# Optimization experiments

Hardware: AMD Instinct MI355X
Metric: run time of the kernel (lower is better)

Reference implementation:

```python
import jax, jax.numpy as jnp
import numpy as np

D_MODEL = 512
N = 2048
BS = 8


def setup_inputs() -> dict:
    key = jax.random.key(0)
    ks = jax.random.split(key, 5)
    inputs1 = jax.random.normal(ks[0], (BS, N, D_MODEL), dtype=jnp.float32)
    inputs2 = jax.random.normal(ks[1], (BS, N, D_MODEL), dtype=jnp.float32)
    # torch Linear weights: init.normal_(std=0.001), bias=0
    Wq = 0.001 * jax.random.normal(ks[2], (D_MODEL, D_MODEL), dtype=jnp.float32)
    Wk = 0.001 * jax.random.normal(ks[3], (D_MODEL, D_MODEL), dtype=jnp.float32)
    Wv = 0.001 * jax.random.normal(ks[4], (D_MODEL, D_MODEL), dtype=jnp.float32)
    bq = jnp.zeros((D_MODEL,), dtype=jnp.float32)
    bk = jnp.zeros((D_MODEL,), dtype=jnp.float32)
    bv = jnp.zeros((D_MODEL,), dtype=jnp.float32)
    # nn.Parameter(torch.ones((n, n)))
    position_biases = jnp.ones((N, N), dtype=jnp.float32)
    return {"inputs1": inputs1, "inputs2": inputs2, "Wq": Wq, "bq": bq,
            "Wk": Wk, "bk": bk, "Wv": Wv, "bv": bv,
            "position_biases": position_biases}


def reference(inputs1, inputs2, Wq, bq, Wk, bk, Wv, bv, position_biases):
    # torch Linear: y = x @ W.T + b
    q = inputs1 @ Wq.T + bq                     # [b, n, d]
    k = inputs1 @ Wk.T + bk                     # [b, s, d]
    v = inputs2 @ Wv.T + bv                     # [b, s, d]
    # exp(k[b,s,d] + bias[t,s]) = exp(bias)[t,s] * exp(k)[b,s,d] -> separable,
    # avoiding the original's (n, bs, n, dim) broadcast intermediate.
    expB = jnp.exp(position_biases)             # [t, s]
    ek = jnp.exp(k)                             # [b, s, d]
    num = jnp.einsum('ts,bsd->btd', expB, ek * v)
    den = jnp.einsum('ts,bsd->btd', expB, ek)
    return jax.nn.sigmoid(q) * (num / den)      # [b, n, d]
```

## Files before the change

### kernel.cpp

```cpp
#include <hip/hip_runtime.h>

typedef float  f32x4  __attribute__((ext_vector_type(4)));
typedef __bf16 bf16x8 __attribute__((ext_vector_type(8)));
typedef __bf16 bf16x4 __attribute__((ext_vector_type(4)));
typedef __bf16 bf16x2 __attribute__((ext_vector_type(2)));

#define D_MODEL 512
#define SEQ     2048
#define BATCH   8
#define ROWS    (BATCH * SEQ)

#define ASYNC_COPY16(dst_lds, src_glb)                                          \
  __builtin_amdgcn_global_load_lds(                                             \
      (const __attribute__((address_space(1))) void*)(src_glb),                 \
      (__attribute__((address_space(3))) void*)(dst_lds), 16, 0, 0)

__global__ void cvt_all_kernel(const float* __restrict__ x1,
                               const float* __restrict__ x2,
                               const float* __restrict__ posb,
                               const float* __restrict__ Wq,
                               const float* __restrict__ Wk,
                               const float* __restrict__ Wv,
                               const float* __restrict__ bq,
                               const float* __restrict__ bk,
                               const float* __restrict__ bv,
                               __bf16* __restrict__ x1b, __bf16* __restrict__ x2b,
                               __bf16* __restrict__ expBb, __bf16* __restrict__ wb,
                               float* __restrict__ bcat)
{
  const int blk = blockIdx.x;
  if (blk < 16384) {
    const float* in = (blk < 8192) ? x1 : x2;
    __bf16* out = (blk < 8192) ? x1b : x2b;
    const int i = (blk & 8191) * 256 + threadIdx.x;
    float4 v = ((const float4*)in)[i];
    bf16x4 o = { (__bf16)v.x, (__bf16)v.y, (__bf16)v.z, (__bf16)v.w };
    ((bf16x4*)out)[i] = o;
  } else if (blk < 20480) {
    const int i = (blk - 16384) * 256 + threadIdx.x;
    float4 v = ((const float4*)posb)[i];
    bf16x4 o = { (__bf16)__expf(v.x), (__bf16)__expf(v.y),
                 (__bf16)__expf(v.z), (__bf16)__expf(v.w) };
    ((bf16x4*)expBb)[i] = o;
  } else if (blk < 21248) {
    const int i = (blk - 20480) * 256 + threadIdx.x;
    const int nW4 = D_MODEL * D_MODEL / 4;
    const float* src = (i < nW4) ? Wq : (i < 2 * nW4) ? Wk : Wv;
    const int ii = i - ((i < nW4) ? 0 : (i < 2 * nW4) ? nW4 : 2 * nW4);
    float4 v = ((const float4*)src)[ii];
    bf16x4 o = { (__bf16)v.x, (__bf16)v.y, (__bf16)v.z, (__bf16)v.w };
    ((bf16x4*)wb)[i] = o;
  } else {
    const int t = (blk - 21248) * 256 + threadIdx.x;
    float v = (t < 512) ? bq[t] : (t < 1024) ? bk[t - 512] : bv[t - 1024];
    bcat[t] = v;
  }
}

__global__ __launch_bounds__(256) void qkv_gemm_kernel(
    const __bf16* __restrict__ x1b, const __bf16* __restrict__ x2b,
    const __bf16* __restrict__ wb, const float* __restrict__ bcat,
    __bf16* __restrict__ sigq, __bf16* __restrict__ kb,
    __bf16* __restrict__ vb)
{
  __shared__ __align__(16) __bf16 As[128 * 64];
  __shared__ __align__(16) __bf16 Bs[128 * 64];

  const int K = D_MODEL;
  const int tid  = threadIdx.x;
  const int wave = tid >> 6;
  const int lane = tid & 63;
  const int quad = lane >> 4;
  const int l16  = lane & 15;
  const int wm   = (wave >> 1) * 64;
  const int wn   = (wave & 1) * 64;
  const int m0 = blockIdx.x * 128;
  const int n0 = blockIdx.y * 128;
  const int l8r = lane >> 3;
  const int scol = ((lane & 7) ^ l8r) * 8;

  const __bf16* A = (blockIdx.y < 8) ? x1b : x2b;

  const __bf16* ga[4]; const __bf16* gb[4];
  __bf16* la[4]; __bf16* lb[4];
  #pragma unroll
  for (int i = 0; i < 4; ++i) {
    ga[i] = A  + (long long)(m0 + i * 32 + wave * 8 + l8r) * K + scol;
    gb[i] = wb + (long long)(n0 + i * 32 + wave * 8 + l8r) * K + scol;
    la[i] = As + (i * 32 + wave * 8) * 64;
    lb[i] = Bs + (i * 32 + wave * 8) * 64;
  }

  f32x4 acc[4][4];
  #pragma unroll
  for (int i = 0; i < 4; ++i)
    #pragma unroll
    for (int j = 0; j < 4; ++j) acc[i][j] = (f32x4){0.f, 0.f, 0.f, 0.f};

  for (int k0 = 0; k0 < K; k0 += 64) {
    #pragma unroll
    for (int i = 0; i < 4; ++i) {
      ASYNC_COPY16(la[i], ga[i] + k0);
      ASYNC_COPY16(lb[i], gb[i] + k0);
    }
    __syncthreads();
    #pragma unroll
    for (int kk = 0; kk < 2; ++kk) {
      const int slot = ((quad + kk * 4) ^ (l16 & 7)) * 8;
      bf16x8 af[4], bfr[4];
      #pragma unroll
      for (int i = 0; i < 4; ++i)
        af[i] = *(const bf16x8*)&As[(wm + i * 16 + l16) * 64 + slot];
      #pragma unroll
      for (int j = 0; j < 4; ++j)
        bfr[j] = *(const bf16x8*)&Bs[(wn + j * 16 + l16) * 64 + slot];
      #pragma unroll
      for (int i = 0; i < 4; ++i)
        #pragma unroll
        for (int j = 0; j < 4; ++j)
          acc[i][j] = __builtin_amdgcn_mfma_f32_16x16x32_bf16(af[i], bfr[j],
                                                              acc[i][j], 0, 0, 0);
    }
    __syncthreads();
  }

  #pragma unroll
  for (int j = 0; j < 4; ++j) {
    const int col = n0 + wn + j * 16 + l16;
    const float bvv = bcat[col];
    #pragma unroll
    for (int i = 0; i < 4; ++i) {
      #pragma unroll
      for (int r = 0; r < 4; ++r) {
        const int row = m0 + wm + i * 16 + quad * 4 + r;
        float x = acc[i][j][r] + bvv;
        if (col < D_MODEL) {
          sigq[(long long)row * D_MODEL + col] = (__bf16)(1.f / (1.f + __expf(-x)));
        } else if (col < 2 * D_MODEL) {
          kb[(long long)row * D_MODEL + (col - D_MODEL)] = (__bf16)x;
        } else {
          vb[(long long)row * D_MODEL + (col - 2 * D_MODEL)] = (__bf16)x;
        }
      }
    }
  }
}

__global__ __launch_bounds__(256) void transform_transpose_kernel(
    const __bf16* __restrict__ kb, const __bf16* __restrict__ vb,
    __bf16* __restrict__ ekvT)
{
  __shared__ float t_ekv[64][67];
  __shared__ float t_ek[64][67];
  const int b  = blockIdx.z;
  const int s0 = blockIdx.x * 64;
  const int d0 = blockIdx.y * 64;
  const int tx = threadIdx.x;
  const int ty = threadIdx.y;
  const __bf16* kp = kb + (long long)b * SEQ * D_MODEL;
  const __bf16* vp = vb + (long long)b * SEQ * D_MODEL;

  #pragma unroll
  for (int it = 0; it < 8; ++it) {
    const int sl = ty + it * 8;
    const long long base = (long long)(s0 + sl) * D_MODEL + d0 + 2 * tx;
    bf16x2 kk2 = *(const bf16x2*)(kp + base);
    bf16x2 vv2 = *(const bf16x2*)(vp + base);
    float e0 = __expf((float)kk2[0]);
    float e1 = __expf((float)kk2[1]);
    t_ek[sl][2 * tx]      = e0;
    t_ek[sl][2 * tx + 1]  = e1;
    t_ekv[sl][2 * tx]     = e0 * (float)vv2[0];
    t_ekv[sl][2 * tx + 1] = e1 * (float)vv2[1];
  }
  __syncthreads();

  __bf16* outp = ekvT + (long long)b * (2 * D_MODEL) * SEQ;
  #pragma unroll
  for (int it = 0; it < 8; ++it) {
    const int dl = ty + it * 8;
    const int d  = d0 + dl;
    const int gr = (d >> 5) * 64 + (d & 31);
    bf16x2 ev = { (__bf16)t_ekv[2 * tx][dl], (__bf16)t_ekv[2 * tx + 1][dl] };
    bf16x2 ee = { (__bf16)t_ek[2 * tx][dl],  (__bf16)t_ek[2 * tx + 1][dl] };
    *(bf16x2*)(outp + (long long)gr * SEQ + s0 + 2 * tx)        = ev;
    *(bf16x2*)(outp + (long long)(gr + 32) * SEQ + s0 + 2 * tx) = ee;
  }
}

__global__ __launch_bounds__(256) void einsum_fused_kernel(
    const __bf16* __restrict__ A, const __bf16* __restrict__ BtAll,
    const __bf16* __restrict__ sigq, float* __restrict__ out)
{
  __shared__ __align__(16) __bf16 As[128 * 64];
  __shared__ __align__(16) __bf16 Bs[128 * 64];

  const int b = blockIdx.z;
  const __bf16* Bt = BtAll + (long long)b * (2 * D_MODEL) * SEQ;
  const int K = SEQ;

  const int tid  = threadIdx.x;
  const int wave = tid >> 6;
  const int lane = tid & 63;
  const int quad = lane >> 4;
  const int l16  = lane & 15;
  const int wm   = (wave >> 1) * 64;
  const int wn   = (wave & 1) * 64;
  const int m0 = blockIdx.x * 128;
  const int n0 = blockIdx.y * 128;
  const int l8r = lane >> 3;
  const int scol = ((lane & 7) ^ l8r) * 8;

  const __bf16* ga[4]; const __bf16* gb[4];
  __bf16* la[4]; __bf16* lb[4];
  #pragma unroll
  for (int i = 0; i < 4; ++i) {
    ga[i] = A  + (long long)(m0 + i * 32 + wave * 8 + l8r) * K + scol;
    gb[i] = Bt + (long long)(n0 + i * 32 + wave * 8 + l8r) * K + scol;
    la[i] = As + (i * 32 + wave * 8) * 64;
    lb[i] = Bs + (i * 32 + wave * 8) * 64;
  }

  f32x4 acc[4][4];
  #pragma unroll
  for (int i = 0; i < 4; ++i)
    #pragma unroll
    for (int j = 0; j < 4; ++j) acc[i][j] = (f32x4){0.f, 0.f, 0.f, 0.f};

  for (int k0 = 0; k0 < K; k0 += 64) {
    #pragma unroll
    for (int i = 0; i < 4; ++i) {
      ASYNC_COPY16(la[i], ga[i] + k0);
      ASYNC_COPY16(lb[i], gb[i] + k0);
    }
    __syncthreads();

    #pragma unroll
    for (int kk = 0; kk < 2; ++kk) {
      const int slot = ((quad + kk * 4) ^ (l16 & 7)) * 8;
      bf16x8 af[4], bfr[4];
      #pragma unroll
      for (int i = 0; i < 4; ++i)
        af[i] = *(const bf16x8*)&As[(wm + i * 16 + l16) * 64 + slot];
      #pragma unroll
      for (int j = 0; j < 4; ++j)
        bfr[j] = *(const bf16x8*)&Bs[(wn + j * 16 + l16) * 64 + slot];
      #pragma unroll
      for (int i = 0; i < 4; ++i)
        #pragma unroll
        for (int j = 0; j < 4; ++j)
          acc[i][j] = __builtin_amdgcn_mfma_f32_16x16x32_bf16(af[i], bfr[j],
                                                              acc[i][j], 0, 0, 0);
    }
    __syncthreads();
  }

  const int g = (n0 + wn) >> 6;
  #pragma unroll
  for (int j = 0; j < 2; ++j) {
    const int d = g * 32 + j * 16 + l16;
    #pragma unroll
    for (int i = 0; i < 4; ++i) {
      #pragma unroll
      for (int r = 0; r < 4; ++r) {
        const int row = m0 + wm + i * 16 + quad * 4 + r;
        const long long off = ((long long)b * SEQ + row) * D_MODEL + d;
        const float num = acc[i][j][r];
        const float den = acc[i][j + 2][r];
        out[off] = (float)sigq[off] * (num / den);
      }
    }
  }
}

extern "C" void kernel_launch(void* const* d_in, const int* in_sizes, int n_in,
                              void* d_out, int out_size, void* d_ws, size_t ws_size,
                              hipStream_t stream) {
  const float* inputs1 = (const float*)d_in[0];
  const float* inputs2 = (const float*)d_in[1];
  const float* Wq = (const float*)d_in[2];
  const float* bq = (const float*)d_in[3];
  const float* Wk = (const float*)d_in[4];
  const float* bk = (const float*)d_in[5];
  const float* Wv = (const float*)d_in[6];
  const float* bv = (const float*)d_in[7];
  const float* posb = (const float*)d_in[8];
  float* out = (float*)d_out;

  char* ws = (char*)d_ws;
  const long long szX  = (long long)ROWS * D_MODEL * 2;
  const long long szW  = (long long)D_MODEL * D_MODEL * 2;
  const long long szEB = (long long)SEQ * SEQ * 2;
  const long long szT  = (long long)BATCH * 2 * D_MODEL * SEQ * 2;
  __bf16* x1b   = (__bf16*)(ws);                 ws += szX;
  __bf16* x2b   = (__bf16*)(ws);                 ws += szX;
  __bf16* wb    = (__bf16*)(ws);                 ws += 3 * szW;
  float*  bcat  = (float*)(ws);                  ws += 3 * D_MODEL * 4;
  __bf16* expBb = (__bf16*)(ws);                 ws += szEB;
  __bf16* sigq  = (__bf16*)(ws);                 ws += szX;
  __bf16* kb    = (__bf16*)(ws);                 ws += szX;
  __bf16* vb    = (__bf16*)(ws);                 ws += szX;
  __bf16* ekvT  = (__bf16*)(ws);                 ws += szT;

  cvt_all_kernel<<<21254, 256, 0, stream>>>(inputs1, inputs2, posb,
                                            Wq, Wk, Wv, bq, bk, bv,
                                            x1b, x2b, expBb, wb, bcat);

  {
    dim3 g(ROWS / 128, (3 * D_MODEL) / 128, 1);
    qkv_gemm_kernel<<<g, 256, 0, stream>>>(x1b, x2b, wb, bcat, sigq, kb, vb);
  }

  {
    dim3 g(SEQ / 64, D_MODEL / 64, BATCH);
    dim3 blk(32, 8, 1);
    transform_transpose_kernel<<<g, blk, 0, stream>>>(kb, vb, ekvT);
  }

  {
    dim3 g(SEQ / 128, (2 * D_MODEL) / 128, BATCH);
    einsum_fused_kernel<<<g, 256, 0, stream>>>(expBb, ekvT, sigq, out);
  }
}
```

Before: 270.5 us.

## Compute K and V projections transposed in GEMM, replace transpose kernel with streaming combine

The QKV GEMM is restructured so that K and V are computed as W·X^T, which writes them directly in a [d, rows] transposed layout. This lets the shared-memory transpose kernel be replaced by a simple vectorized elementwise combine that computes exp(k) and exp(k)*v. Each GEMM block now handles two tiles, with the next tile's first stage prefetched across the tile boundary. Biases are read directly and the separate bias-concatenation pass is dropped. The trade-off is that the transposed epilogue writes are strided 2-byte stores, which may coalesce poorly.

```diff
diff --git a/kernel.cpp b/kernel.cpp
--- a/kernel.cpp
+++ b/kernel.cpp
@@ -3,7 +3,6 @@
 typedef float  f32x4  __attribute__((ext_vector_type(4)));
 typedef __bf16 bf16x8 __attribute__((ext_vector_type(8)));
 typedef __bf16 bf16x4 __attribute__((ext_vector_type(4)));
-typedef __bf16 bf16x2 __attribute__((ext_vector_type(2)));
 
 #define D_MODEL 512
 #define SEQ     2048
@@ -21,12 +20,8 @@
                                const float* __restrict__ Wq,
                                const float* __restrict__ Wk,
                                const float* __restrict__ Wv,
-                               const float* __restrict__ bq,
-                               const float* __restrict__ bk,
-                               const float* __restrict__ bv,
                                __bf16* __restrict__ x1b, __bf16* __restrict__ x2b,
-                               __bf16* __restrict__ expBb, __bf16* __restrict__ wb,
-                               float* __restrict__ bcat)
+                               __bf16* __restrict__ expBb, __bf16* __restrict__ wb)
 {
   const int blk = blockIdx.x;
   if (blk < 16384) {
@@ -42,7 +37,7 @@
     bf16x4 o = { (__bf16)__expf(v.x), (__bf16)__expf(v.y),
                  (__bf16)__expf(v.z), (__bf16)__expf(v.w) };
     ((bf16x4*)expBb)[i] = o;
-  } else if (blk < 21248) {
+  } else {
     const int i = (blk - 20480) * 256 + threadIdx.x;
     const int nW4 = D_MODEL * D_MODEL / 4;
     const float* src = (i < nW4) ? Wq : (i < 2 * nW4) ? Wk : Wv;
@@ -50,23 +45,22 @@
     float4 v = ((const float4*)src)[ii];
     bf16x4 o = { (__bf16)v.x, (__bf16)v.y, (__bf16)v.z, (__bf16)v.w };
     ((bf16x4*)wb)[i] = o;
-  } else {
-    const int t = (blk - 21248) * 256 + threadIdx.x;
-    float v = (t < 512) ? bq[t] : (t < 1024) ? bk[t - 512] : bv[t - 1024];
-    bcat[t] = v;
-  }
-}
-
-__global__ __launch_bounds__(256) void qkv_gemm_kernel(
+  }
+}
+
+__global__ __launch_bounds__(256) void tri_gemm_kernel(
     const __bf16* __restrict__ x1b, const __bf16* __restrict__ x2b,
-    const __bf16* __restrict__ wb, const float* __restrict__ bcat,
-    __bf16* __restrict__ sigq, __bf16* __restrict__ kb,
-    __bf16* __restrict__ vb)
+    const __bf16* __restrict__ wb,
+    const float* __restrict__ bq, const float* __restrict__ bk,
+    const float* __restrict__ bv,
+    __bf16* __restrict__ sigq, __bf16* __restrict__ kT,
+    __bf16* __restrict__ vT)
 {
   __shared__ __align__(16) __bf16 As[128 * 64];
   __shared__ __align__(16) __bf16 Bs[128 * 64];
 
   const int K = D_MODEL;
+  const int z = blockIdx.z;
   const int tid  = threadIdx.x;
   const int wave = tid >> 6;
   const int lane = tid & 63;
@@ -74,118 +68,135 @@
   const int l16  = lane & 15;
   const int wm   = (wave >> 1) * 64;
   const int wn   = (wave & 1) * 64;
-  const int m0 = blockIdx.x * 128;
-  const int n0 = blockIdx.y * 128;
   const int l8r = lane >> 3;
   const int scol = ((lane & 7) ^ l8r) * 8;
-
-  const __bf16* A = (blockIdx.y < 8) ? x1b : x2b;
+  const int F0 = blockIdx.y * 128;
+
+  const __bf16* Ap = (z == 0) ? x1b
+                   : (z == 1) ? (wb + (long long)D_MODEL * D_MODEL)
+                              : (wb + 2LL * D_MODEL * D_MODEL);
+  const __bf16* Bp = (z == 0) ? wb : (z == 1) ? x1b : x2b;
+
+  const int srow = wave * 8 + l8r;
 
   const __bf16* ga[4]; const __bf16* gb[4];
-  __bf16* la[4]; __bf16* lb[4];
-  #pragma unroll
-  for (int i = 0; i < 4; ++i) {
-    ga[i] = A  + (long long)(m0 + i * 32 + wave * 8 + l8r) * K + scol;
-    gb[i] = wb + (long long)(n0 + i * 32 + wave * 8 + l8r) * K + scol;
-    la[i] = As + (i * 32 + wave * 8) * 64;
-    lb[i] = Bs + (i * 32 + wave * 8) * 64;
-  }
-
-  f32x4 acc[4][4];
-  #pragma unroll
-  for (int i = 0; i < 4; ++i)
-    #pragma unroll
-    for (int j = 0; j < 4; ++j) acc[i][j] = (f32x4){0.f, 0.f, 0.f, 0.f};
-
-  for (int k0 = 0; k0 < K; k0 += 64) {
+  auto set_tile = [&](int t) {
+    const int L0 = (blockIdx.x * 2 + t) * 128;
+    const int m0 = (z == 0) ? L0 : F0;
+    const int n0 = (z == 0) ? F0 : L0;
     #pragma unroll
     for (int i = 0; i < 4; ++i) {
-      ASYNC_COPY16(la[i], ga[i] + k0);
-      ASYNC_COPY16(lb[i], gb[i] + k0);
-    }
-    __syncthreads();
-    #pragma unroll
-    for (int kk = 0; kk < 2; ++kk) {
-      const int slot = ((quad + kk * 4) ^ (l16 & 7)) * 8;
-      bf16x8 af[4], bfr[4];
-      #pragma unroll
-      for (int i = 0; i < 4; ++i)
-        af[i] = *(const bf16x8*)&As[(wm + i * 16 + l16) * 64 + slot];
-      #pragma unroll
-      for (int j = 0; j < 4; ++j)
-        bfr[j] = *(const bf16x8*)&Bs[(wn + j * 16 + l16) * 64 + slot];
-      #pragma unroll
-      for (int i = 0; i < 4; ++i)
+      ga[i] = Ap + (long long)(m0 + i * 32 + srow) * K + scol;
+      gb[i] = Bp + (long long)(n0 + i * 32 + srow) * K + scol;
+    }
+  };
+  auto stage = [&](int k0) {
+    #pragma unroll
+    for (int i = 0; i < 4; ++i) {
+      ASYNC_COPY16(As + (i * 32 + wave * 8) * 64, ga[i] + k0);
+      ASYNC_COPY16(Bs + (i * 32 + wave * 8) * 64, gb[i] + k0);
+    }
+  };
+
+  set_tile(0);
+  stage(0);
+
+  for (int t = 0; t < 2; ++t) {
+    f32x4 acc[4][4];
+    #pragma unroll
+    for (int i = 0; i < 4; ++i)
+      #pragma unroll
+      for (int j = 0; j < 4; ++j) acc[i][j] = (f32x4){0.f, 0.f, 0.f, 0.f};
+
+    for (int k0 = 0; k0 < K; k0 += 64) {
+      __syncthreads();
+      #pragma unroll
+      for (int kk = 0; kk < 2; ++kk) {
+        const int slot = ((quad + kk * 4) ^ (l16 & 7)) * 8;
+        bf16x8 af[4], bfr[4];
+        #pragma unroll
+        for (int i = 0; i < 4; ++i)
+          af[i] = *(const bf16x8*)&As[(wm + i * 16 + l16) * 64 + slot];
         #pragma unroll
         for (int j = 0; j < 4; ++j)
-          acc[i][j] = __builtin_amdgcn_mfma_f32_16x16x32_bf16(af[i], bfr[j],
-                                                              acc[i][j], 0, 0, 0);
-    }
-    __syncthreads();
-  }
-
-  #pragma unroll
-  for (int j = 0; j < 4; ++j) {
-    const int col = n0 + wn + j * 16 + l16;
-    const float bvv = bcat[col];
-    #pragma unroll
-    for (int i = 0; i < 4; ++i) {
-      #pragma unroll
-      for (int r = 0; r < 4; ++r) {
-        const int row = m0 + wm + i * 16 + quad * 4 + r;
-        float x = acc[i][j][r] + bvv;
-        if (col < D_MODEL) {
-          sigq[(long long)row * D_MODEL + col] = (__bf16)(1.f / (1.f + __expf(-x)));
-        } else if (col < 2 * D_MODEL) {
-          kb[(long long)row * D_MODEL + (col - D_MODEL)] = (__bf16)x;
-        } else {
-          vb[(long long)row * D_MODEL + (col - 2 * D_MODEL)] = (__bf16)x;
+          bfr[j] = *(const bf16x8*)&Bs[(wn + j * 16 + l16) * 64 + slot];
+        #pragma unroll
+        for (int i = 0; i < 4; ++i)
+          #pragma unroll
+          for (int j = 0; j < 4; ++j)
+            acc[i][j] = __builtin_amdgcn_mfma_f32_16x16x32_bf16(af[i], bfr[j],
+                                                                acc[i][j], 0, 0, 0);
+      }
+      __syncthreads();
+      if (k0 + 64 < K) {
+        stage(k0 + 64);
+      } else if (t == 0) {
+        set_tile(1);
+        stage(0);
+      }
+    }
+
+    const int L0 = (blockIdx.x * 2 + t) * 128;
+    if (z == 0) {
+      const int m0 = L0, n0 = F0;
+      #pragma unroll
+      for (int j = 0; j < 4; ++j) {
+        const int col = n0 + wn + j * 16 + l16;
+        const float bvv = bq[col];
+        #pragma unroll
+        for (int i = 0; i < 4; ++i)
+          #pragma unroll
+          for (int r = 0; r < 4; ++r) {
+            const int row = m0 + wm + i * 16 + quad * 4 + r;
+            float x = acc[i][j][r] + bvv;
+            sigq[(long long)row * D_MODEL + col] =
+                (__bf16)(1.f / (1.f + __expf(-x)));
+          }
+      }
+    } else {
+      const int m0 = F0, n0 = L0;
+      const float* bias = (z == 1) ? bk : bv;
+      __bf16* outp = (z == 1) ? kT : vT;
+      #pragma unroll
+      for (int i = 0; i < 4; ++i) {
+        #pragma unroll
+        for (int r = 0; r < 4; ++r) {
+          const int d = m0 + wm + i * 16 + quad * 4 + r;
+          const float bvv = bias[d];
+          #pragma unroll
+          for (int j = 0; j < 4; ++j) {
+            const int rr = n0 + wn + j * 16 + l16;
+            outp[(long long)d * ROWS + rr] = (__bf16)(acc[i][j][r] + bvv);
+          }
         }
       }
     }
   }
 }
 
-__global__ __launch_bounds__(256) void transform_transpose_kernel(
-    const __bf16* __restrict__ kb, const __bf16* __restrict__ vb,
+__global__ __launch_bounds__(256) void combine_kernel(
+    const __bf16* __restrict__ kT, const __bf16* __restrict__ vT,
     __bf16* __restrict__ ekvT)
 {
-  __shared__ float t_ekv[64][67];
-  __shared__ float t_ek[64][67];
-  const int b  = blockIdx.z;
-  const int s0 = blockIdx.x * 64;
-  const int d0 = blockIdx.y * 64;
-  const int tx = threadIdx.x;
-  const int ty = threadIdx.y;
-  const __bf16* kp = kb + (long long)b * SEQ * D_MODEL;
-  const __bf16* vp = vb + (long long)b * SEQ * D_MODEL;
-
+  const int c = blockIdx.x * 256 + threadIdx.x;
+  const int d   = c >> 11;
+  const int off = (c & 2047) * 8;
+  const int b = off >> 11;
+  const int s = off & 2047;
+
+  bf16x8 kk = *(const bf16x8*)(kT + (long long)d * ROWS + off);
+  bf16x8 vv = *(const bf16x8*)(vT + (long long)d * ROWS + off);
+  bf16x8 ek, ev;
   #pragma unroll
-  for (int it = 0; it < 8; ++it) {
-    const int sl = ty + it * 8;
-    const long long base = (long long)(s0 + sl) * D_MODEL + d0 + 2 * tx;
-    bf16x2 kk2 = *(const bf16x2*)(kp + base);
-    bf16x2 vv2 = *(const bf16x2*)(vp + base);
-    float e0 = __expf((float)kk2[0]);
-    float e1 = __expf((float)kk2[1]);
-    t_ek[sl][2 * tx]      = e0;
-    t_ek[sl][2 * tx + 1]  = e1;
-    t_ekv[sl][2 * tx]     = e0 * (float)vv2[0];
-    t_ekv[sl][2 * tx + 1] = e1 * (float)vv2[1];
-  }
-  __syncthreads();
-
-  __bf16* outp = ekvT + (long long)b * (2 * D_MODEL) * SEQ;
-  #pragma unroll
-  for (int it = 0; it < 8; ++it) {
-    const int dl = ty + it * 8;
-    const int d  = d0 + dl;
-    const int gr = (d >> 5) * 64 + (d & 31);
-    bf16x2 ev = { (__bf16)t_ekv[2 * tx][dl], (__bf16)t_ekv[2 * tx + 1][dl] };
-    bf16x2 ee = { (__bf16)t_ek[2 * tx][dl],  (__bf16)t_ek[2 * tx + 1][dl] };
-    *(bf16x2*)(outp + (long long)gr * SEQ + s0 + 2 * tx)        = ev;
-    *(bf16x2*)(outp + (long long)(gr + 32) * SEQ + s0 + 2 * tx) = ee;
-  }
+  for (int e = 0; e < 8; ++e) {
+    float ekf = __expf((float)kk[e]);
+    ek[e] = (__bf16)ekf;
+    ev[e] = (__bf16)(ekf * (float)vv[e]);
+  }
+  const int gr = ((d >> 5) << 6) + (d & 31);
+  __bf16* outp = ekvT + (long long)b * (2 * D_MODEL) * SEQ + s;
+  *(bf16x8*)(outp + (long long)gr * SEQ)        = ev;
+  *(bf16x8*)(outp + (long long)(gr + 32) * SEQ) = ek;
 }
 
 __global__ __launch_bounds__(256) void einsum_fused_kernel(
@@ -295,27 +306,23 @@
   __bf16* x1b   = (__bf16*)(ws);                 ws += szX;
   __bf16* x2b   = (__bf16*)(ws);                 ws += szX;
   __bf16* wb    = (__bf16*)(ws);                 ws += 3 * szW;
-  float*  bcat  = (float*)(ws);                  ws += 3 * D_MODEL * 4;
   __bf16* expBb = (__bf16*)(ws);                 ws += szEB;
   __bf16* sigq  = (__bf16*)(ws);                 ws += szX;
-  __bf16* kb    = (__bf16*)(ws);                 ws += szX;
-  __bf16* vb    = (__bf16*)(ws);                 ws += szX;
+  __bf16* kT    = (__bf16*)(ws);                 ws += szX;
+  __bf16* vT    = (__bf16*)(ws);                 ws += szX;
   __bf16* ekvT  = (__bf16*)(ws);                 ws += szT;
 
-  cvt_all_kernel<<<21254, 256, 0, stream>>>(inputs1, inputs2, posb,
-                                            Wq, Wk, Wv, bq, bk, bv,
-                                            x1b, x2b, expBb, wb, bcat);
+  cvt_all_kernel<<<21248, 256, 0, stream>>>(inputs1, inputs2, posb,
+                                            Wq, Wk, Wv,
+                                            x1b, x2b, expBb, wb);
 
   {
-    dim3 g(ROWS / 128, (3 * D_MODEL) / 128, 1);
-    qkv_gemm_kernel<<<g, 256, 0, stream>>>(x1b, x2b, wb, bcat, sigq, kb, vb);
-  }
-
-  {
-    dim3 g(SEQ / 64, D_MODEL / 64, BATCH);
-    dim3 blk(32, 8, 1);
-    transform_transpose_kernel<<<g, blk, 0, stream>>>(kb, vb, ekvT);
-  }
+    dim3 g(ROWS / 256, D_MODEL / 128, 3);
+    tri_gemm_kernel<<<g, 256, 0, stream>>>(x1b, x2b, wb, bq, bk, bv,
+                                           sigq, kT, vT);
+  }
+
+  combine_kernel<<<(D_MODEL * ROWS / 8) / 256, 256, 0, stream>>>(kT, vT, ekvT);
 
   {
     dim3 g(SEQ / 128, (2 * D_MODEL) / 128, BATCH);
```

Result: faster. 264.2 us (-2.3%).
